# Kernel optimization log

Hardware: AMD Instinct MI355X
Metric: run time of the kernel (lower is better)

Reference implementation:

```python
import jax, jax.numpy as jnp
import numpy as np

BN_EPS = 1e-5


def setup_inputs() -> dict:
    key = jax.random.key(0)
    ks = jax.random.split(key, 4)
    B, C, H, W = 4, 256, 64, 64
    Ck, Cv = 64, 256
    x = jax.random.normal(ks[0], (B, C, H, W), dtype=jnp.float32)
    Wk = jax.random.normal(ks[1], (Ck, C), dtype=jnp.float32) * (1.0 / np.sqrt(C))
    bk = jax.random.normal(ks[2], (Ck,), dtype=jnp.float32) * 0.02
    Wv = jax.random.normal(ks[3], (Cv, C), dtype=jnp.float32) * (1.0 / np.sqrt(C))
    bv = jnp.zeros((Cv,), dtype=jnp.float32)
    return {
        "x": x,
        "Wk": Wk,
        "bk": bk,
        "bn_gamma": jnp.ones((Ck,), dtype=jnp.float32),
        "bn_beta": jnp.zeros((Ck,), dtype=jnp.float32),
        "bn_mean": jnp.zeros((Ck,), dtype=jnp.float32),
        "bn_var": jnp.ones((Ck,), dtype=jnp.float32),
        "Wv": Wv,
        "bv": bv,
    }


def reference(x, Wk, bk, bn_gamma, bn_beta, bn_mean, bn_var, Wv, bv):
    B, C, H, W = x.shape
    HW = H * W
    # 1x1 conv == channel matmul; f_query = f_key (shared weights), so Q == K
    k = jnp.einsum("bchw,kc->bkhw", x, Wk) + bk[None, :, None, None]
    # BatchNorm2d (inference mode: running stats)
    inv = bn_gamma * jax.lax.rsqrt(bn_var + BN_EPS)
    k = k * inv[None, :, None, None] + (bn_beta - bn_mean * inv)[None, :, None, None]
    k = k.reshape(B, -1, HW)                      # [B, Ck, HW]
    v = (jnp.einsum("bchw,kc->bkhw", x, Wv) + bv[None, :, None, None]).reshape(B, -1, HW)  # [B, Cv, HW]
    # energy[b,i,j] = sum_c Q[b,c,i] * K[b,c,j]  (no scaling, as in source)
    energy = jnp.einsum("bci,bcj->bij", k, k)     # [B, HW, HW]
    attn = jax.nn.softmax(energy, axis=-1)
    # out[b,c,i] = sum_j V[b,c,j] * attn[i,j]
    out = jnp.einsum("bcj,bij->bci", v, attn)
    return out.reshape(B, -1, H, W)
```

## Files before the change

### kernel.cpp

```cpp
#include <hip/hip_runtime.h>
#include <math.h>

#define BN_EPS 1e-5f

constexpr int B  = 4;
constexpr int C  = 256;
constexpr int HW = 4096;
constexpr int CK = 64;
constexpr int CV = 256;
constexpr int CO = 320;
constexpr int CHG = 2;

typedef short bf16x8 __attribute__((ext_vector_type(8)));
typedef float f32x4  __attribute__((ext_vector_type(4)));

__device__ __forceinline__ ushort f2bf(float f) {
    unsigned u = __float_as_uint(f);
    u += 0x7FFFu + ((u >> 16) & 1u);
    return (ushort)(u >> 16);
}

__device__ __forceinline__ int swzk(int r) {
    return (((r & 3) | ((((r >> 2) ^ (r >> 3)) & 1) << 2)) << 4);
}
__device__ __forceinline__ int swzv(int r) { return (r & 7) << 4; }

__device__ __forceinline__ void gload_lds16(const void* g, void* l) {
    __builtin_amdgcn_global_load_lds(
        (const __attribute__((address_space(1))) unsigned*)g,
        (__attribute__((address_space(3))) unsigned*)l, 16, 0, 0);
}

__global__ __launch_bounds__(256) void wprep(
    const float* __restrict__ Wk, const float* __restrict__ bk,
    const float* __restrict__ gamma, const float* __restrict__ beta,
    const float* __restrict__ mean,  const float* __restrict__ var,
    const float* __restrict__ Wv, const float* __restrict__ bv,
    ushort* __restrict__ Wq, float* __restrict__ bq)
{
    const int co = blockIdx.x;
    const int c  = threadIdx.x;
    float w;
    if (co < CK) {
        float inv = gamma[co] * rsqrtf(var[co] + BN_EPS);
        w = Wk[co * C + c] * inv;
        if (c == 0) bq[co] = bk[co] * inv + (beta[co] - mean[co] * inv);
    } else {
        w = Wv[(co - CK) * C + c];
        if (c == 0) bq[co] = bv[co - CK];
    }
    const int wv  = co / 80, rem = co % 80;
    const int mi  = rem / 16, colw = rem % 16;
    const int ks  = c >> 5, qw = (c >> 3) & 3, e = c & 7;
    Wq[((((((wv * 8 + ks) * 5 + mi) * 4 + qw) * 16 + colw)) << 3) + e] = f2bf(w);
}

__global__ __launch_bounds__(256) void kv_gemm(
    const float* __restrict__ x, const ushort* __restrict__ Wq,
    const float* __restrict__ bq,
    ushort* __restrict__ Kbuf, ushort* __restrict__ Vbuf,
    float* __restrict__ mb, unsigned* __restrict__ Mx)
{
    __shared__ __align__(16) ushort xt[32][C + 8];

    const int t    = threadIdx.x;
    const int lane = t & 63;
    const int wv   = t >> 6;
    const int q    = lane >> 4;
    const int col  = lane & 15;
    const int hw0  = blockIdx.x * 32;
    const int b    = blockIdx.y;

    const float* xb = x + (size_t)b * C * HW;

    {
        const int cq  = (t >> 5) * 4;
        const int hwo = t & 31;
#pragma unroll
        for (int pass = 0; pass < 8; pass++) {
            const int c0 = pass * 32;
            float a0 = xb[(size_t)(c0 + cq + 0) * HW + hw0 + hwo];
            float a1 = xb[(size_t)(c0 + cq + 1) * HW + hw0 + hwo];
            float a2 = xb[(size_t)(c0 + cq + 2) * HW + hw0 + hwo];
            float a3 = xb[(size_t)(c0 + cq + 3) * HW + hw0 + hwo];
            ushort4 u = make_ushort4(f2bf(a0), f2bf(a1), f2bf(a2), f2bf(a3));
            *(ushort4*)&xt[hwo][c0 + cq] = u;
        }
    }
    __syncthreads();

    f32x4 acc[5][2];
#pragma unroll
    for (int mi = 0; mi < 5; mi++)
#pragma unroll
        for (int nt = 0; nt < 2; nt++)
            acc[mi][nt] = (f32x4){0.f, 0.f, 0.f, 0.f};

#pragma unroll
    for (int ks = 0; ks < 8; ks++) {
        bf16x8 av[5], bvv[2];
#pragma unroll
        for (int mi = 0; mi < 5; mi++)
            av[mi] = *(const bf16x8*)(Wq + ((size_t)((wv * 8 + ks) * 5 + mi) << 9) + lane * 8);
#pragma unroll
        for (int nt = 0; nt < 2; nt++)
            bvv[nt] = *(const bf16x8*)&xt[nt * 16 + col][ks * 32 + q * 8];
#pragma unroll
        for (int mi = 0; mi < 5; mi++)
#pragma unroll
            for (int nt = 0; nt < 2; nt++)
                acc[mi][nt] = __builtin_amdgcn_mfma_f32_16x16x32_bf16(av[mi], bvv[nt], acc[mi][nt], 0, 0, 0);
    }

    float ssq[2] = {0.f, 0.f};
#pragma unroll
    for (int mi = 0; mi < 5; mi++) {
        const int cot = wv * 80 + mi * 16;
        float bi[4];
#pragma unroll
        for (int r = 0; r < 4; r++) bi[r] = bq[cot + q * 4 + r];
#pragma unroll
        for (int nt = 0; nt < 2; nt++) {
            const int hw = hw0 + nt * 16 + col;
            float v0 = acc[mi][nt][0] + bi[0];
            float v1 = acc[mi][nt][1] + bi[1];
            float v2 = acc[mi][nt][2] + bi[2];
            float v3 = acc[mi][nt][3] + bi[3];
            if (cot < CK) {
                ushort4 kk = make_ushort4(f2bf(v0), f2bf(v1), f2bf(v2), f2bf(v3));
                *(ushort4*)&Kbuf[((size_t)b * HW + hw) * CK + cot + q * 4] = kk;
                ssq[nt] += v0 * v0 + v1 * v1 + v2 * v2 + v3 * v3;
            } else {
                const int cv = cot - CK + q * 4;
                Vbuf[((size_t)b * CV + cv + 0) * HW + hw] = f2bf(v0);
                Vbuf[((size_t)b * CV + cv + 1) * HW + hw] = f2bf(v1);
                Vbuf[((size_t)b * CV + cv + 2) * HW + hw] = f2bf(v2);
                Vbuf[((size_t)b * CV + cv + 3) * HW + hw] = f2bf(v3);
            }
        }
    }

    if (wv == 0) {
        float mxn = 0.f;
#pragma unroll
        for (int nt = 0; nt < 2; nt++) {
            float ss = ssq[nt];
            ss += __shfl_xor(ss, 16, 64);
            ss += __shfl_xor(ss, 32, 64);
            float nr = sqrtf(ss);
            if (lane < 16) mb[(size_t)b * HW + hw0 + nt * 16 + col] = nr;
            mxn = fmaxf(mxn, nr);
        }
#pragma unroll
        for (int off = 1; off <= 32; off <<= 1)
            mxn = fmaxf(mxn, __shfl_xor(mxn, off, 64));
        if (t == 0) atomicMax(Mx + b, __float_as_uint(mxn));
    }
}

#define PACKP(S, W0, W1, LACC, MV)                                             \
    {                                                                          \
        _Pragma("unroll")                                                      \
        for (int nt = 0; nt < 4; nt++) {                                       \
            float p0 = __expf(S[nt][0] - MV);                                  \
            float p1 = __expf(S[nt][1] - MV);                                  \
            float p2 = __expf(S[nt][2] - MV);                                  \
            float p3 = __expf(S[nt][3] - MV);                                  \
            LACC += (p0 + p1) + (p2 + p3);                                     \
            if (nt == 0) {                                                     \
                W0[0] = (short)f2bf(p0); W0[1] = (short)f2bf(p1);              \
                W0[2] = (short)f2bf(p2); W0[3] = (short)f2bf(p3);              \
            } else if (nt == 1) {                                              \
                W0[4] = (short)f2bf(p0); W0[5] = (short)f2bf(p1);              \
                W0[6] = (short)f2bf(p2); W0[7] = (short)f2bf(p3);              \
            } else if (nt == 2) {                                              \
                W1[0] = (short)f2bf(p0); W1[1] = (short)f2bf(p1);              \
                W1[2] = (short)f2bf(p2); W1[3] = (short)f2bf(p3);              \
            } else {                                                           \
                W1[4] = (short)f2bf(p0); W1[5] = (short)f2bf(p1);              \
                W1[6] = (short)f2bf(p2); W1[7] = (short)f2bf(p3);              \
            }                                                                  \
        }                                                                      \
    }

__global__ __launch_bounds__(256, 1) void attn_kernel(
    const ushort* __restrict__ Kbuf, const ushort* __restrict__ Vbuf,
    const float* __restrict__ mb, const unsigned* __restrict__ Mx,
    float* __restrict__ out)
{
    __shared__ __align__(16) ushort Kt[2][64 * 64];
    __shared__ __align__(16) ushort Vt[2][128 * 64];

    const int t    = threadIdx.x;
    const int lane = t & 63;
    const int wv   = t >> 6;
    const int q    = lane >> 4;
    const int col  = lane & 15;

    const unsigned lin = blockIdx.x + 32u * (blockIdx.y + 2u * blockIdx.z);
    const int xcd   = lin & 7;
    const int s_    = lin >> 3;
    const int i0g   = s_ * 128;
    const int chg   = xcd & 1;
    const int b     = xcd >> 1;

    const int iw    = wv * 16 + col;
    const int jperm = (col >> 2) * 8 + (col & 3);

    const ushort* Kb = Kbuf + (size_t)b * HW * CK;
    const ushort* Vb = Vbuf + (size_t)b * CV * HW;
    const int cbase = chg * 128;

    bf16x8 qaA[2], qaB[2];
#pragma unroll
    for (int k = 0; k < 2; k++) {
        qaA[k] = *(const bf16x8*)(Kb + (size_t)(i0g + iw) * CK + k * 32 + q * 8);
        qaB[k] = *(const bf16x8*)(Kb + (size_t)(i0g + 64 + iw) * CK + k * 32 + q * 8);
    }

    const float Mxf = __uint_as_float(Mx[b]);
    const float mA = mb[(size_t)b * HW + i0g + iw] * Mxf;
    const float mB = mb[(size_t)b * HW + i0g + 64 + iw] * Mxf;

    f32x4 OA[8], OB[8];
#pragma unroll
    for (int mt = 0; mt < 8; mt++) {
        OA[mt] = (f32x4){0.f, 0.f, 0.f, 0.f};
        OB[mt] = (f32x4){0.f, 0.f, 0.f, 0.f};
    }

    float lA = 0.f, lB = 0.f;
    const f32x4 zf = (f32x4){0.f, 0.f, 0.f, 0.f};

#define STAGE(BUF, JN)                                                         \
    {                                                                          \
        const int jn_s = (JN);                                                 \
        _Pragma("unroll")                                                      \
        for (int p = 0; p < 2; p++) {                                          \
            int off = (wv * 2 + p) * 1024 + lane * 16;                         \
            int r = off >> 7, cb = off & 127;                                  \
            const char* g = (const char*)Kb + (size_t)(jn_s + r) * 128         \
                            + (cb ^ swzk(r));                                  \
            gload_lds16(g, (char*)&Kt[BUF][0] + off);                          \
        }                                                                      \
        _Pragma("unroll")                                                      \
        for (int p = 0; p < 4; p++) {                                          \
            int off = (wv * 4 + p) * 1024 + lane * 16;                         \
            int r = off >> 7, cb = off & 127;                                  \
            const char* g = (const char*)Vb                                    \
                            + ((size_t)(cbase + r) * HW + jn_s) * 2            \
                            + (cb ^ swzv(r));                                  \
            gload_lds16(g, (char*)&Vt[BUF][0] + off);                          \
        }                                                                      \
    }

    STAGE(0, 0);
    __syncthreads();

    int cur = 0;
    for (int j0 = 0; j0 < HW; j0 += 64) {
        STAGE(cur ^ 1, (j0 + 64) & (HW - 1));

        const char* KtB = (const char*)&Kt[cur][0];
        const char* VtB = (const char*)&Vt[cur][0];

        f32x4 SA[4], SB[4];
        __builtin_amdgcn_s_setprio(1);
#pragma unroll
        for (int nt = 0; nt < 4; nt++) {
            const int jr = jperm + (nt >> 1) * 32 + (nt & 1) * 4;
            bf16x8 k0 = *(const bf16x8*)(KtB + jr * 128 + ((q * 16) ^ swzk(jr)));
            bf16x8 k1 = *(const bf16x8*)(KtB + jr * 128 + ((64 + q * 16) ^ swzk(jr)));
            SA[nt] = __builtin_amdgcn_mfma_f32_16x16x32_bf16(k0, qaA[0], zf, 0, 0, 0);
            SA[nt] = __builtin_amdgcn_mfma_f32_16x16x32_bf16(k1, qaA[1], SA[nt], 0, 0, 0);
            SB[nt] = __builtin_amdgcn_mfma_f32_16x16x32_bf16(k0, qaB[0], zf, 0, 0, 0);
            SB[nt] = __builtin_amdgcn_mfma_f32_16x16x32_bf16(k1, qaB[1], SB[nt], 0, 0, 0);
        }
        __builtin_amdgcn_s_setprio(0);

        bf16x8 wA0, wA1, wB0, wB1;
        PACKP(SA, wA0, wA1, lA, mA);
        PACKP(SB, wB0, wB1, lB, mB);

        __builtin_amdgcn_s_setprio(1);
#pragma unroll
        for (int mt = 0; mt < 8; mt++) {
            const int vr = mt * 16 + col;
            bf16x8 v0 = *(const bf16x8*)(VtB + vr * 128 + ((q * 16) ^ swzv(vr)));
            bf16x8 v1 = *(const bf16x8*)(VtB + vr * 128 + ((64 + q * 16) ^ swzv(vr)));
            OA[mt] = __builtin_amdgcn_mfma_f32_16x16x32_bf16(v0, wA0, OA[mt], 0, 0, 0);
            OA[mt] = __builtin_amdgcn_mfma_f32_16x16x32_bf16(v1, wA1, OA[mt], 0, 0, 0);
            OB[mt] = __builtin_amdgcn_mfma_f32_16x16x32_bf16(v0, wB0, OB[mt], 0, 0, 0);
            OB[mt] = __builtin_amdgcn_mfma_f32_16x16x32_bf16(v1, wB1, OB[mt], 0, 0, 0);
        }
        __builtin_amdgcn_s_setprio(0);

        __syncthreads();
        cur ^= 1;
    }
#undef STAGE

    lA += __shfl_xor(lA, 16, 64);
    lA += __shfl_xor(lA, 32, 64);
    lB += __shfl_xor(lB, 16, 64);
    lB += __shfl_xor(lB, 32, 64);
    const float invA = 1.0f / lA;
    const float invB = 1.0f / lB;

    float* ob = out + (size_t)b * CV * HW;
#pragma unroll
    for (int mt = 0; mt < 8; mt++)
#pragma unroll
        for (int r = 0; r < 4; r++) {
            const size_t c = cbase + mt * 16 + q * 4 + r;
            ob[c * HW + i0g + iw]      = OA[mt][r] * invA;
            ob[c * HW + i0g + 64 + iw] = OB[mt][r] * invB;
        }
}

extern "C" void kernel_launch(void* const* d_in, const int* in_sizes, int n_in,
                              void* d_out, int out_size, void* d_ws, size_t ws_size,
                              hipStream_t stream)
{
    const float* x     = (const float*)d_in[0];
    const float* Wk    = (const float*)d_in[1];
    const float* bk    = (const float*)d_in[2];
    const float* gamma = (const float*)d_in[3];
    const float* beta  = (const float*)d_in[4];
    const float* mean  = (const float*)d_in[5];
    const float* var   = (const float*)d_in[6];
    const float* Wv    = (const float*)d_in[7];
    const float* bv    = (const float*)d_in[8];
    float* out = (float*)d_out;

    ushort*   Kbuf = (ushort*)d_ws;
    ushort*   Vbuf = Kbuf + (size_t)B * HW * CK;
    ushort*   Wq   = Vbuf + (size_t)B * CV * HW;
    float*    bq   = (float*)(Wq + (size_t)CO * C);
    float*    mb   = bq + CO;
    unsigned* Mx   = (unsigned*)(mb + (size_t)B * HW);

    hipMemsetAsync(Mx, 0, B * sizeof(unsigned), stream);

    wprep<<<dim3(CO), 256, 0, stream>>>(Wk, bk, gamma, beta, mean, var, Wv, bv, Wq, bq);

    kv_gemm<<<dim3(HW / 32, B), 256, 0, stream>>>(x, Wq, bq, Kbuf, Vbuf, mb, Mx);

    dim3 g2(HW / 128, CHG, B);
    attn_kernel<<<g2, 256, 0, stream>>>(Kbuf, Vbuf, mb, Mx, out);
}
```

Measured before the change: 197.5 us.

## Split attention key range across blocks with atomic accumulation and normalization pass

The attention kernel's key/value sequence is split into two halves handled by separate blocks. This doubles the grid and raises occupancy to two blocks per CU. Partial outputs and softmax row sums are accumulated with float atomics into zeroed buffers, and a new kernel then divides by the sums. The shared global max-norm bound is used for the exponentials, so partials combine without rescaling. The kv_gemm MFMA operand order is also swapped, so V stores are vectorized while K stores become scalar. The cost is an output memset, atomic traffic on the full output tensor, and an extra read/write pass.

```diff
diff --git a/kernel.cpp b/kernel.cpp
--- a/kernel.cpp
+++ b/kernel.cpp
@@ -10,6 +10,7 @@
 constexpr int CV = 256;
 constexpr int CO = 320;
 constexpr int CHG = 2;
+constexpr int JS  = 2;
 
 typedef short bf16x8 __attribute__((ext_vector_type(8)));
 typedef float f32x4  __attribute__((ext_vector_type(4)));
@@ -109,33 +110,33 @@
         for (int mi = 0; mi < 5; mi++)
 #pragma unroll
             for (int nt = 0; nt < 2; nt++)
-                acc[mi][nt] = __builtin_amdgcn_mfma_f32_16x16x32_bf16(av[mi], bvv[nt], acc[mi][nt], 0, 0, 0);
-    }
-
-    float ssq[2] = {0.f, 0.f};
+                acc[mi][nt] = __builtin_amdgcn_mfma_f32_16x16x32_bf16(bvv[nt], av[mi], acc[mi][nt], 0, 0, 0);
+    }
+
+    float ssq[2][4] = {{0.f,0.f,0.f,0.f},{0.f,0.f,0.f,0.f}};
 #pragma unroll
     for (int mi = 0; mi < 5; mi++) {
         const int cot = wv * 80 + mi * 16;
-        float bi[4];
-#pragma unroll
-        for (int r = 0; r < 4; r++) bi[r] = bq[cot + q * 4 + r];
+        const float bi = bq[cot + col];
 #pragma unroll
         for (int nt = 0; nt < 2; nt++) {
-            const int hw = hw0 + nt * 16 + col;
-            float v0 = acc[mi][nt][0] + bi[0];
-            float v1 = acc[mi][nt][1] + bi[1];
-            float v2 = acc[mi][nt][2] + bi[2];
-            float v3 = acc[mi][nt][3] + bi[3];
+            const int hwr = hw0 + nt * 16 + q * 4;
+            float v0 = acc[mi][nt][0] + bi;
+            float v1 = acc[mi][nt][1] + bi;
+            float v2 = acc[mi][nt][2] + bi;
+            float v3 = acc[mi][nt][3] + bi;
             if (cot < CK) {
-                ushort4 kk = make_ushort4(f2bf(v0), f2bf(v1), f2bf(v2), f2bf(v3));
-                *(ushort4*)&Kbuf[((size_t)b * HW + hw) * CK + cot + q * 4] = kk;
-                ssq[nt] += v0 * v0 + v1 * v1 + v2 * v2 + v3 * v3;
+                const int ck = cot + col;
+                Kbuf[((size_t)b * HW + hwr + 0) * CK + ck] = f2bf(v0);
+                Kbuf[((size_t)b * HW + hwr + 1) * CK + ck] = f2bf(v1);
+                Kbuf[((size_t)b * HW + hwr + 2) * CK + ck] = f2bf(v2);
+                Kbuf[((size_t)b * HW + hwr + 3) * CK + ck] = f2bf(v3);
+                ssq[nt][0] += v0 * v0; ssq[nt][1] += v1 * v1;
+                ssq[nt][2] += v2 * v2; ssq[nt][3] += v3 * v3;
             } else {
-                const int cv = cot - CK + q * 4;
-                Vbuf[((size_t)b * CV + cv + 0) * HW + hw] = f2bf(v0);
-                Vbuf[((size_t)b * CV + cv + 1) * HW + hw] = f2bf(v1);
-                Vbuf[((size_t)b * CV + cv + 2) * HW + hw] = f2bf(v2);
-                Vbuf[((size_t)b * CV + cv + 3) * HW + hw] = f2bf(v3);
+                const int cv = cot - CK + col;
+                ushort4 vv = make_ushort4(f2bf(v0), f2bf(v1), f2bf(v2), f2bf(v3));
+                *(ushort4*)&Vbuf[((size_t)b * CV + cv) * HW + hwr] = vv;
             }
         }
     }
@@ -144,12 +145,16 @@
         float mxn = 0.f;
 #pragma unroll
         for (int nt = 0; nt < 2; nt++) {
-            float ss = ssq[nt];
-            ss += __shfl_xor(ss, 16, 64);
-            ss += __shfl_xor(ss, 32, 64);
-            float nr = sqrtf(ss);
-            if (lane < 16) mb[(size_t)b * HW + hw0 + nt * 16 + col] = nr;
-            mxn = fmaxf(mxn, nr);
+#pragma unroll
+            for (int off = 1; off <= 8; off <<= 1)
+#pragma unroll
+                for (int r = 0; r < 4; r++)
+                    ssq[nt][r] += __shfl_xor(ssq[nt][r], off, 64);
+            float4 nr = make_float4(sqrtf(ssq[nt][0]), sqrtf(ssq[nt][1]),
+                                    sqrtf(ssq[nt][2]), sqrtf(ssq[nt][3]));
+            if (col == 0)
+                *(float4*)&mb[(size_t)b * HW + hw0 + nt * 16 + q * 4] = nr;
+            mxn = fmaxf(mxn, fmaxf(fmaxf(nr.x, nr.y), fmaxf(nr.z, nr.w)));
         }
 #pragma unroll
         for (int off = 1; off <= 32; off <<= 1)
@@ -183,10 +188,10 @@
         }                                                                      \
     }
 
-__global__ __launch_bounds__(256, 1) void attn_kernel(
+__global__ __launch_bounds__(256, 2) void attn_kernel(
     const ushort* __restrict__ Kbuf, const ushort* __restrict__ Vbuf,
     const float* __restrict__ mb, const unsigned* __restrict__ Mx,
-    float* __restrict__ out)
+    float* __restrict__ out, float* __restrict__ Lbuf)
 {
     __shared__ __align__(16) ushort Kt[2][64 * 64];
     __shared__ __align__(16) ushort Vt[2][128 * 64];
@@ -197,13 +202,16 @@
     const int q    = lane >> 4;
     const int col  = lane & 15;
 
-    const unsigned lin = blockIdx.x + 32u * (blockIdx.y + 2u * blockIdx.z);
+    const unsigned lin = blockIdx.x + 32u * (blockIdx.y + 4u * blockIdx.z);
     const int xcd   = lin & 7;
     const int s_    = lin >> 3;
-    const int i0g   = s_ * 128;
-    const int chg   = xcd & 1;
-    const int b     = xcd >> 1;
-
+    const int combo = xcd + 8 * (s_ >> 5);
+    const int i0g   = (s_ & 31) * 128;
+    const int chg   = combo & 1;
+    const int js    = (combo >> 1) & 1;
+    const int b     = combo >> 2;
+
+    const int jbase = js * (HW / JS);
     const int iw    = wv * 16 + col;
     const int jperm = (col >> 2) * 8 + (col & 3);
 
@@ -254,12 +262,12 @@
         }                                                                      \
     }
 
-    STAGE(0, 0);
+    STAGE(0, jbase);
     __syncthreads();
 
     int cur = 0;
-    for (int j0 = 0; j0 < HW; j0 += 64) {
-        STAGE(cur ^ 1, (j0 + 64) & (HW - 1));
+    for (int jo = 0; jo < HW / JS; jo += 64) {
+        STAGE(cur ^ 1, jbase + ((jo + 64) & (HW / JS - 1)));
 
         const char* KtB = (const char*)&Kt[cur][0];
         const char* VtB = (const char*)&Vt[cur][0];
@@ -304,8 +312,10 @@
     lA += __shfl_xor(lA, 32, 64);
     lB += __shfl_xor(lB, 16, 64);
     lB += __shfl_xor(lB, 32, 64);
-    const float invA = 1.0f / lA;
-    const float invB = 1.0f / lB;
+    if (chg == 0 && q == 0) {
+        atomicAdd(Lbuf + (size_t)b * HW + i0g + iw,      lA);
+        atomicAdd(Lbuf + (size_t)b * HW + i0g + 64 + iw, lB);
+    }
 
     float* ob = out + (size_t)b * CV * HW;
 #pragma unroll
@@ -313,9 +323,22 @@
 #pragma unroll
         for (int r = 0; r < 4; r++) {
             const size_t c = cbase + mt * 16 + q * 4 + r;
-            ob[c * HW + i0g + iw]      = OA[mt][r] * invA;
-            ob[c * HW + i0g + 64 + iw] = OB[mt][r] * invB;
-        }
+            atomicAdd(&ob[c * HW + i0g + iw],      OA[mt][r]);
+            atomicAdd(&ob[c * HW + i0g + 64 + iw], OB[mt][r]);
+        }
+}
+
+__global__ __launch_bounds__(256) void norm_out(
+    float* __restrict__ out, const float* __restrict__ Lbuf)
+{
+    const int g    = blockIdx.x * 256 + threadIdx.x;
+    const int flat = g * 4;
+    const int i    = flat & (HW - 1);
+    const int b    = flat >> 20;
+    float4 o = *(float4*)&out[flat];
+    const float4 l4 = *(const float4*)&Lbuf[(size_t)b * HW + i];
+    o.x /= l4.x; o.y /= l4.y; o.z /= l4.z; o.w /= l4.w;
+    *(float4*)&out[flat] = o;
 }
 
 extern "C" void kernel_launch(void* const* d_in, const int* in_sizes, int n_in,
@@ -338,14 +361,19 @@
     ushort*   Wq   = Vbuf + (size_t)B * CV * HW;
     float*    bq   = (float*)(Wq + (size_t)CO * C);
     float*    mb   = bq + CO;
-    unsigned* Mx   = (unsigned*)(mb + (size_t)B * HW);
+    float*    Lbuf = mb + (size_t)B * HW;
+    unsigned* Mx   = (unsigned*)(Lbuf + (size_t)B * HW);
 
     hipMemsetAsync(Mx, 0, B * sizeof(unsigned), stream);
+    hipMemsetAsync(Lbuf, 0, (size_t)B * HW * sizeof(float), stream);
+    hipMemsetAsync(out, 0, (size_t)out_size * sizeof(float), stream);
 
     wprep<<<dim3(CO), 256, 0, stream>>>(Wk, bk, gamma, beta, mean, var, Wv, bv, Wq, bq);
 
     kv_gemm<<<dim3(HW / 32, B), 256, 0, stream>>>(x, Wq, bq, Kbuf, Vbuf, mb, Mx);
 
-    dim3 g2(HW / 128, CHG, B);
-    attn_kernel<<<g2, 256, 0, stream>>>(Kbuf, Vbuf, mb, Mx, out);
-}
+    dim3 g2(HW / 128, CHG * JS, B);
+    attn_kernel<<<g2, 256, 0, stream>>>(Kbuf, Vbuf, mb, Mx, out, Lbuf);
+
+    norm_out<<<dim3(out_size / 4 / 256), 256, 0, stream>>>(out, Lbuf);
+}
```

After: 191.3 us. 3.1% less time.
